# Optimization experiments

Hardware: AMD Instinct MI355X
Metric: run time of the kernel (lower is better)

## Reference

```python
import jax, jax.numpy as jnp
import numpy as np
from math import sqrt

HEADS = 16
DIM_HEAD = 64
BETA = 1.0 / sqrt(DIM_HEAD)


def setup_inputs() -> dict:
    key = jax.random.key(0)
    k1, k2, k3 = jax.random.split(key, 3)
    b, n, dim = 2, 2048, 1024
    inner = HEADS * DIM_HEAD  # 1024
    x = jax.random.normal(k1, (b, n, dim), dtype=jnp.float32)
    W_qk = jax.random.normal(k2, (dim, 2 * inner), dtype=jnp.float32) * 0.02
    W_out = jax.random.normal(k3, (inner, dim), dtype=jnp.float32) * 0.02
    return {"x": x, "W_qk": W_qk, "W_out": W_out}


def reference(x, W_qk, W_out):
    # x: [b, n, dim]; to_qk: Linear(dim, 2*inner, bias=False)
    b, n, _ = x.shape
    qk = x @ W_qk                                   # [b, n, 2*inner]
    q, k = jnp.split(qk, 2, axis=-1)                # each [b, n, inner]
    # b n (h d) -> b h n d
    q = q.reshape(b, n, HEADS, DIM_HEAD).transpose(0, 2, 1, 3)
    k = k.reshape(b, n, HEADS, DIM_HEAD).transpose(0, 2, 1, 3)
    # beta-scaled scores
    scores = jnp.einsum('bhid,bhjd->bhij', q * BETA, k)  # [b, h, n, n]
    mask_value = -jnp.finfo(scores.dtype).max
    causal_mask = jnp.triu(jnp.ones((n, n), dtype=bool), k=1)
    scores = jnp.where(causal_mask, mask_value, scores)
    attn = jax.nn.softmax(scores, axis=-1)
    # K is reused as V
    out = jnp.einsum('bhij,bhjd->bhid', attn, k)    # [b, h, n, d]
    out = out.transpose(0, 2, 1, 3).reshape(b, n, HEADS * DIM_HEAD)
    # to_out Linear (dropout is identity in eval)
    return out @ W_out
```

## Files before the change

kernel.cpp:

```cpp
#include <hip/hip_runtime.h>
#include <hip/hip_bf16.h>
#include <math.h>

typedef short bf16x8 __attribute__((ext_vector_type(8)));
typedef float f32x4 __attribute__((ext_vector_type(4)));

__device__ __forceinline__ float bf2f(unsigned short u) {
    return __uint_as_float(((unsigned int)u) << 16);
}
__device__ __forceinline__ unsigned short f2bf(float f) {
    unsigned int u = __float_as_uint(f);
    u = (u + 0x7FFFu + ((u >> 16) & 1u)) >> 16;
    return (unsigned short)u;
}
__device__ __forceinline__ unsigned int pk2bf(float a, float b) {
    __hip_bfloat162 u = __float22bfloat162_rn(make_float2(a, b));
    return *(unsigned int*)&u;
}

#define ASYNC16(gp, lp)                                                        \
    __builtin_amdgcn_global_load_lds(                                          \
        (const __attribute__((address_space(1))) unsigned int*)(gp),           \
        (__attribute__((address_space(3))) unsigned int*)(lp), 16, 0, 0)

__global__ __launch_bounds__(256) void wtrans_kernel(const float* __restrict__ Wqk,
                                                     const float* __restrict__ Wout,
                                                     unsigned short* __restrict__ Wqk_t,
                                                     unsigned short* __restrict__ Wout_t) {
    const int z = blockIdx.z;
    const int N = z ? 1024 : 2048;
    if (z && blockIdx.y >= 32) return;
    const float* in = z ? Wout : Wqk;
    unsigned short* out = z ? Wout_t : Wqk_t;
    const int K = 1024;
    __shared__ float tile[32][33];
    int k0 = blockIdx.x * 32, n0 = blockIdx.y * 32;
    int tx = threadIdx.x & 31, ty = threadIdx.x >> 5;
    #pragma unroll
    for (int i = ty; i < 32; i += 8)
        tile[i][tx] = in[(size_t)(k0 + i) * N + (n0 + tx)];
    __syncthreads();
    #pragma unroll
    for (int i = ty; i < 32; i += 8)
        out[(size_t)(n0 + i) * K + (k0 + tx)] = f2bf(tile[tx][i]);
}

template <bool STORE_BF16, bool A_FP32, bool WRITE_KT>
__global__ __launch_bounds__(256) void gemm12864_kernel(const void* __restrict__ Av,
                                                        const unsigned short* __restrict__ Bt,
                                                        void* __restrict__ C,
                                                        unsigned short* __restrict__ kT,
                                                        int K, int lda, int ldb, int ldc) {
    constexpr int ASTR = A_FP32 ? 40 : 32;
    __shared__ unsigned short As[128 * ASTR];
    __shared__ unsigned short Bs[64 * 32];
    const int tid = threadIdx.x;
    const int wave = tid >> 6;
    const int lane = tid & 63;
    const int quad = lane >> 4;
    const int col  = lane & 15;
    const int wm = (wave >> 1) * 64;
    const int wn = (wave & 1) * 32;
    const int m0 = blockIdx.x * 128, n0 = blockIdx.y * 64;

    f32x4 acc[4][2];
    #pragma unroll
    for (int i = 0; i < 4; ++i)
        #pragma unroll
        for (int j = 0; j < 2; ++j) { acc[i][j][0] = 0.f; acc[i][j][1] = 0.f; acc[i][j][2] = 0.f; acc[i][j][3] = 0.f; }

    const int srow = tid >> 2;
    const int skc  = (tid & 3) * 8;
    const int frow = tid >> 1;
    const int fcol = (tid & 1) * 16;

    for (int k0 = 0; k0 < K; k0 += 32) {
        __syncthreads();
        if (A_FP32) {
            const float* gx = (const float*)Av + (size_t)(m0 + frow) * lda + k0 + fcol;
            float4 f0 = *(const float4*)(gx);
            float4 f1 = *(const float4*)(gx + 4);
            float4 f2 = *(const float4*)(gx + 8);
            float4 f3 = *(const float4*)(gx + 12);
            uint4 w0 = make_uint4(pk2bf(f0.x, f0.y), pk2bf(f0.z, f0.w),
                                  pk2bf(f1.x, f1.y), pk2bf(f1.z, f1.w));
            uint4 w1 = make_uint4(pk2bf(f2.x, f2.y), pk2bf(f2.z, f2.w),
                                  pk2bf(f3.x, f3.y), pk2bf(f3.z, f3.w));
            *(uint4*)&As[frow * ASTR + fcol]     = w0;
            *(uint4*)&As[frow * ASTR + fcol + 8] = w1;
        } else {
            const unsigned short* ga = (const unsigned short*)Av + (size_t)(m0 + srow) * lda + k0 + skc;
            ASYNC16(ga,            &As[wave * 512]);
            ASYNC16(ga + 64 * lda, &As[2048 + wave * 512]);
        }
        const unsigned short* gb = Bt + (size_t)(n0 + srow) * ldb + k0 + skc;
        ASYNC16(gb, &Bs[wave * 512]);
        __syncthreads();

        bf16x8 af[4], bf[2];
        #pragma unroll
        for (int mf = 0; mf < 4; ++mf)
            af[mf] = *(const bf16x8*)&As[(wm + mf * 16 + col) * ASTR + quad * 8];
        #pragma unroll
        for (int nf = 0; nf < 2; ++nf)
            bf[nf] = *(const bf16x8*)&Bs[(wn + nf * 16 + col) * 32 + quad * 8];
        #pragma unroll
        for (int mf = 0; mf < 4; ++mf)
            #pragma unroll
            for (int nf = 0; nf < 2; ++nf)
                acc[mf][nf] = __builtin_amdgcn_mfma_f32_16x16x32_bf16(af[mf], bf[nf], acc[mf][nf], 0, 0, 0);
    }

    #pragma unroll
    for (int mf = 0; mf < 4; ++mf) {
        const int row0 = m0 + wm + mf * 16 + quad * 4;
        #pragma unroll
        for (int nf = 0; nf < 2; ++nf) {
            const int cc = n0 + wn + nf * 16 + col;
            #pragma unroll
            for (int r = 0; r < 4; ++r) {
                if (STORE_BF16)
                    ((unsigned short*)C)[(size_t)(row0 + r) * ldc + cc] = f2bf(acc[mf][nf][r]);
                else
                    ((float*)C)[(size_t)(row0 + r) * ldc + cc] = acc[mf][nf][r];
            }
            if (WRITE_KT && cc >= 1024) {
                const int bb = row0 >> 11, tok = row0 & 2047;
                ushort4 v;
                v.x = f2bf(acc[mf][nf][0]); v.y = f2bf(acc[mf][nf][1]);
                v.z = f2bf(acc[mf][nf][2]); v.w = f2bf(acc[mf][nf][3]);
                *(ushort4*)(kT + ((size_t)(bb * 1024 + cc - 1024)) * 2048 + tok) = v;
            }
        }
    }
}

#define LDK 72

__global__ __launch_bounds__(256) void attn_v5_kernel(const unsigned short* __restrict__ qkb,
                                                      const unsigned short* __restrict__ kT,
                                                      unsigned short* __restrict__ aout) {
    __shared__ unsigned short Kbuf[2][2][64 * 64];
    __shared__ unsigned short Ps[4][16 * LDK];

    const int bh = blockIdx.x;
    const int b = bh >> 4, h = bh & 15;
    const int qtile = 31 - (int)blockIdx.y;
    const int tid = threadIdx.x;
    const int wave = tid >> 6, lane = tid & 63, quad = lane >> 4, col = lane & 15;

    bf16x8 qa0, qa1;
    {
        const unsigned short* qp =
            qkb + ((size_t)(b * 2048 + qtile * 64 + wave * 16 + col)) * 2048 + h * 64;
        bf16x8 r0 = *(const bf16x8*)(qp + quad * 8);
        bf16x8 r1 = *(const bf16x8*)(qp + 32 + quad * 8);
        const float sc = 0.125f * 1.44269504088896f;
        #pragma unroll
        for (int i = 0; i < 8; ++i) {
            qa0[i] = (short)f2bf(bf2f((unsigned short)r0[i]) * sc);
            qa1[i] = (short)f2bf(bf2f((unsigned short)r1[i]) * sc);
        }
    }

    f32x4 accO[4];
    #pragma unroll
    for (int t = 0; t < 4; ++t) { accO[t][0] = 0.f; accO[t][1] = 0.f; accO[t][2] = 0.f; accO[t][3] = 0.f; }
    float lsum = 0.f;

    const int r8 = lane >> 3;
    const int c8 = (lane & 7) ^ r8;
    const unsigned short* knp =
        qkb + ((size_t)(b * 2048 + wave * 16 + r8)) * 2048 + 1024 + h * 64 + c8 * 8;
    const unsigned short* ktp = kT + ((size_t)(bh * 64 + wave * 16 + r8)) * 2048 + c8 * 8;

    auto issue = [&](int jt, int p) {
        const unsigned short* kn = knp + (size_t)jt * 64 * 2048;
        const unsigned short* kt = ktp + jt * 64;
        unsigned short* knl = &Kbuf[p][0][(wave * 16) * 64];
        unsigned short* ktl = &Kbuf[p][1][(wave * 16) * 64];
        ASYNC16(kn,            knl);
        ASYNC16(kn + 8 * 2048, knl + 8 * 64);
        ASYNC16(kt,            ktl);
        ASYNC16(kt + 8 * 2048, ktl + 8 * 64);
    };

    issue(0, 0);

    for (int jt = 0; jt <= qtile; ++jt) {
        const int cur = jt & 1;
        __builtin_amdgcn_s_barrier();
        if (jt < qtile) issue(jt + 1, cur ^ 1);
        if (jt < qtile) __builtin_amdgcn_s_waitcnt(0xF74);
        else            __builtin_amdgcn_s_waitcnt(0xF70);
        __builtin_amdgcn_s_barrier();
        __asm__ volatile("" ::: "memory");

        const unsigned short* Knc = &Kbuf[cur][0][0];
        const unsigned short* Ktc = &Kbuf[cur][1][0];

        const bool diag = (jt == qtile);
        const int tmax = diag ? wave : 3;

        float ls = 0.f;
        unsigned int pw[4][2];
        #pragma unroll
        for (int t = 0; t < 4; ++t) {
            if (t <= tmax) {
                const int row = (t * 16 + col) * 64;
                const int sw = col & 7;
                bf16x8 ka0 = *(const bf16x8*)&Knc[row + (quad ^ sw) * 8];
                bf16x8 ka1 = *(const bf16x8*)&Knc[row + ((4 + quad) ^ sw) * 8];
                f32x4 c = {-16.f, -16.f, -16.f, -16.f};
                c = __builtin_amdgcn_mfma_f32_16x16x32_bf16(ka0, qa0, c, 0, 0, 0);
                c = __builtin_amdgcn_mfma_f32_16x16x32_bf16(ka1, qa1, c, 0, 0, 0);
                if (diag && t == wave) {
                    #pragma unroll
                    for (int r = 0; r < 4; ++r)
                        if (quad * 4 + r > col) c[r] = -1e30f;
                }
                const float p0 = exp2f(c[0]);
                const float p1 = exp2f(c[1]);
                const float p2 = exp2f(c[2]);
                const float p3 = exp2f(c[3]);
                ls += (p0 + p1) + (p2 + p3);
                pw[t][0] = pk2bf(p0, p1);
                pw[t][1] = pk2bf(p2, p3);
            } else {
                pw[t][0] = 0u; pw[t][1] = 0u;
            }
        }
        lsum += ls;

        unsigned short* psb = &Ps[wave][col * LDK];
        #pragma unroll
        for (int t = 0; t < 4; ++t)
            *(uint2*)(psb + t * 16 + quad * 4) = make_uint2(pw[t][0], pw[t][1]);

        bf16x8 pa0 = *(const bf16x8*)(psb + quad * 8);
        bf16x8 pa1 = *(const bf16x8*)(psb + 32 + quad * 8);
        const bool hi = !(diag && wave < 2);

        #pragma unroll
        for (int t = 0; t < 4; ++t) {
            const int row = (t * 16 + col) * 64;
            const int sw = col & 7;
            bf16x8 vb0 = *(const bf16x8*)&Ktc[row + (quad ^ sw) * 8];
            accO[t] = __builtin_amdgcn_mfma_f32_16x16x32_bf16(pa0, vb0, accO[t], 0, 0, 0);
            if (hi) {
                bf16x8 vb1 = *(const bf16x8*)&Ktc[row + ((4 + quad) ^ sw) * 8];
                accO[t] = __builtin_amdgcn_mfma_f32_16x16x32_bf16(pa1, vb1, accO[t], 0, 0, 0);
            }
        }
    }

    lsum += __shfl_xor(lsum, 16);
    lsum += __shfl_xor(lsum, 32);
    #pragma unroll
    for (int r = 0; r < 4; ++r) {
        const float lr = __shfl(lsum, (lane & 48) | (quad * 4 + r));
        const float inv = 1.f / lr;
        const size_t row = (size_t)b * 2048 + qtile * 64 + wave * 16 + quad * 4 + r;
        unsigned short* op = aout + row * 1024 + h * 64;
        op[col]      = f2bf(accO[0][r] * inv);
        op[16 + col] = f2bf(accO[1][r] * inv);
        op[32 + col] = f2bf(accO[2][r] * inv);
        op[48 + col] = f2bf(accO[3][r] * inv);
    }
}

extern "C" void kernel_launch(void* const* d_in, const int* in_sizes, int n_in,
                              void* d_out, int out_size, void* d_ws, size_t ws_size,
                              hipStream_t stream) {
    (void)in_sizes; (void)n_in; (void)out_size; (void)ws_size;
    const float* x    = (const float*)d_in[0];
    const float* Wqk  = (const float*)d_in[1];
    const float* Wout = (const float*)d_in[2];
    float* out = (float*)d_out;

    unsigned short* kT     = (unsigned short*)d_ws;
    unsigned short* Wqk_t  = kT     + (size_t)2048 * 2048;
    unsigned short* Wout_t = Wqk_t  + (size_t)2048 * 1024;
    unsigned short* qkb    = Wout_t + (size_t)1024 * 1024;
    unsigned short* aoutb  = qkb    + (size_t)4096 * 2048;

    wtrans_kernel<<<dim3(32, 64, 2), dim3(256), 0, stream>>>(Wqk, Wout, Wqk_t, Wout_t);

    gemm12864_kernel<true, true, true><<<dim3(32, 32), dim3(256), 0, stream>>>(
        (const void*)x, Wqk_t, (void*)qkb, kT, 1024, 1024, 1024, 2048);

    attn_v5_kernel<<<dim3(32, 32), dim3(256), 0, stream>>>(qkb, kT, aoutb);

    gemm12864_kernel<false, false, false><<<dim3(32, 16), dim3(256), 0, stream>>>(
        (const void*)aoutb, Wout_t, (void*)out, nullptr, 1024, 1024, 1024, 1024);
}
```

Baseline: 198.3 us.

## Shrink GEMM tiles to 64x64 with register-staged loads and padded LDS

Replaces the 128x64 GEMM tile with a 64x64 tile in which each wave computes a 16x64 strip. Global loads are issued into registers before the barrier and then written to padded LDS (stride 40), replacing the async global-to-LDS path. This doubles the grid size for both projection GEMMs, aiming for better occupancy and latency hiding. In exchange, each MFMA gets less operand reuse and global/LDS traffic per FLOP rises.

```diff
diff --git a/kernel.cpp b/kernel.cpp
--- a/kernel.cpp
+++ b/kernel.cpp
@@ -46,91 +46,71 @@
 }
 
 template <bool STORE_BF16, bool A_FP32, bool WRITE_KT>
-__global__ __launch_bounds__(256) void gemm12864_kernel(const void* __restrict__ Av,
-                                                        const unsigned short* __restrict__ Bt,
-                                                        void* __restrict__ C,
-                                                        unsigned short* __restrict__ kT,
-                                                        int K, int lda, int ldb, int ldc) {
-    constexpr int ASTR = A_FP32 ? 40 : 32;
-    __shared__ unsigned short As[128 * ASTR];
-    __shared__ unsigned short Bs[64 * 32];
-    const int tid = threadIdx.x;
+__global__ __launch_bounds__(256) void gemm64_kernel(const void* __restrict__ Av,
+                                                     const unsigned short* __restrict__ Bt,
+                                                     void* __restrict__ C,
+                                                     unsigned short* __restrict__ kT,
+                                                     int K, int lda, int ldb, int ldc) {
+    __shared__ unsigned short As[64 * 40];
+    __shared__ unsigned short Bs[64 * 40];
+    const int tid  = threadIdx.x;
     const int wave = tid >> 6;
     const int lane = tid & 63;
     const int quad = lane >> 4;
-    const int col  = lane & 15;
-    const int wm = (wave >> 1) * 64;
-    const int wn = (wave & 1) * 32;
-    const int m0 = blockIdx.x * 128, n0 = blockIdx.y * 64;
-
-    f32x4 acc[4][2];
-    #pragma unroll
-    for (int i = 0; i < 4; ++i)
-        #pragma unroll
-        for (int j = 0; j < 2; ++j) { acc[i][j][0] = 0.f; acc[i][j][1] = 0.f; acc[i][j][2] = 0.f; acc[i][j][3] = 0.f; }
-
-    const int srow = tid >> 2;
-    const int skc  = (tid & 3) * 8;
-    const int frow = tid >> 1;
-    const int fcol = (tid & 1) * 16;
+    const int lrow = lane & 15;
+    const int m0 = blockIdx.x * 64;
+    const int n0 = blockIdx.y * 64;
+    const int ar = tid >> 2;
+    const int ac = (tid & 3) * 8;
+
+    f32x4 acc[4];
+    #pragma unroll
+    for (int t = 0; t < 4; ++t) { acc[t][0] = 0.f; acc[t][1] = 0.f; acc[t][2] = 0.f; acc[t][3] = 0.f; }
+
+    const unsigned short* Bp = Bt + (size_t)(n0 + ar) * ldb + ac;
 
     for (int k0 = 0; k0 < K; k0 += 32) {
-        __syncthreads();
+        bf16x8 bv = *(const bf16x8*)(Bp + k0);
         if (A_FP32) {
-            const float* gx = (const float*)Av + (size_t)(m0 + frow) * lda + k0 + fcol;
+            const float* gx = (const float*)Av + (size_t)(m0 + ar) * lda + k0 + ac;
             float4 f0 = *(const float4*)(gx);
             float4 f1 = *(const float4*)(gx + 4);
-            float4 f2 = *(const float4*)(gx + 8);
-            float4 f3 = *(const float4*)(gx + 12);
-            uint4 w0 = make_uint4(pk2bf(f0.x, f0.y), pk2bf(f0.z, f0.w),
-                                  pk2bf(f1.x, f1.y), pk2bf(f1.z, f1.w));
-            uint4 w1 = make_uint4(pk2bf(f2.x, f2.y), pk2bf(f2.z, f2.w),
-                                  pk2bf(f3.x, f3.y), pk2bf(f3.z, f3.w));
-            *(uint4*)&As[frow * ASTR + fcol]     = w0;
-            *(uint4*)&As[frow * ASTR + fcol + 8] = w1;
+            uint4 w = make_uint4(pk2bf(f0.x, f0.y), pk2bf(f0.z, f0.w),
+                                 pk2bf(f1.x, f1.y), pk2bf(f1.z, f1.w));
+            __syncthreads();
+            *(uint4*)&As[ar * 40 + ac] = w;
         } else {
-            const unsigned short* ga = (const unsigned short*)Av + (size_t)(m0 + srow) * lda + k0 + skc;
-            ASYNC16(ga,            &As[wave * 512]);
-            ASYNC16(ga + 64 * lda, &As[2048 + wave * 512]);
-        }
-        const unsigned short* gb = Bt + (size_t)(n0 + srow) * ldb + k0 + skc;
-        ASYNC16(gb, &Bs[wave * 512]);
+            bf16x8 av = *(const bf16x8*)((const unsigned short*)Av + (size_t)(m0 + ar) * lda + k0 + ac);
+            __syncthreads();
+            *(bf16x8*)&As[ar * 40 + ac] = av;
+        }
+        *(bf16x8*)&Bs[ar * 40 + ac] = bv;
         __syncthreads();
-
-        bf16x8 af[4], bf[2];
-        #pragma unroll
-        for (int mf = 0; mf < 4; ++mf)
-            af[mf] = *(const bf16x8*)&As[(wm + mf * 16 + col) * ASTR + quad * 8];
-        #pragma unroll
-        for (int nf = 0; nf < 2; ++nf)
-            bf[nf] = *(const bf16x8*)&Bs[(wn + nf * 16 + col) * 32 + quad * 8];
-        #pragma unroll
-        for (int mf = 0; mf < 4; ++mf)
-            #pragma unroll
-            for (int nf = 0; nf < 2; ++nf)
-                acc[mf][nf] = __builtin_amdgcn_mfma_f32_16x16x32_bf16(af[mf], bf[nf], acc[mf][nf], 0, 0, 0);
-    }
-
-    #pragma unroll
-    for (int mf = 0; mf < 4; ++mf) {
-        const int row0 = m0 + wm + mf * 16 + quad * 4;
-        #pragma unroll
-        for (int nf = 0; nf < 2; ++nf) {
-            const int cc = n0 + wn + nf * 16 + col;
-            #pragma unroll
-            for (int r = 0; r < 4; ++r) {
-                if (STORE_BF16)
-                    ((unsigned short*)C)[(size_t)(row0 + r) * ldc + cc] = f2bf(acc[mf][nf][r]);
-                else
-                    ((float*)C)[(size_t)(row0 + r) * ldc + cc] = acc[mf][nf][r];
-            }
-            if (WRITE_KT && cc >= 1024) {
-                const int bb = row0 >> 11, tok = row0 & 2047;
-                ushort4 v;
-                v.x = f2bf(acc[mf][nf][0]); v.y = f2bf(acc[mf][nf][1]);
-                v.z = f2bf(acc[mf][nf][2]); v.w = f2bf(acc[mf][nf][3]);
-                *(ushort4*)(kT + ((size_t)(bb * 1024 + cc - 1024)) * 2048 + tok) = v;
-            }
+        bf16x8 afrag = *(const bf16x8*)&As[(wave * 16 + lrow) * 40 + quad * 8];
+        #pragma unroll
+        for (int t = 0; t < 4; ++t) {
+            bf16x8 bfrag = *(const bf16x8*)&Bs[(t * 16 + lrow) * 40 + quad * 8];
+            acc[t] = __builtin_amdgcn_mfma_f32_16x16x32_bf16(afrag, bfrag, acc[t], 0, 0, 0);
+        }
+    }
+
+    const int row0 = m0 + wave * 16 + quad * 4;
+    #pragma unroll
+    for (int t = 0; t < 4; ++t) {
+        const int cc = n0 + t * 16 + lrow;
+        #pragma unroll
+        for (int r = 0; r < 4; ++r) {
+            if (STORE_BF16)
+                ((unsigned short*)C)[(size_t)(row0 + r) * ldc + cc] = f2bf(acc[t][r]);
+            else
+                ((float*)C)[(size_t)(row0 + r) * ldc + cc] = acc[t][r];
+        }
+        if (WRITE_KT && cc >= 1024) {
+            const int bb = row0 >> 11, tok = row0 & 2047;
+            ushort4 v;
+            v.x = f2bf(acc[t][0]); v.y = f2bf(acc[t][1]);
+            v.z = f2bf(acc[t][2]); v.w = f2bf(acc[t][3]);
+            *(ushort4*)(kT + ((size_t)(bb * 1024 + cc - 1024)) * 2048 + tok) = v;
         }
     }
 }
@@ -286,11 +266,11 @@
 
     wtrans_kernel<<<dim3(32, 64, 2), dim3(256), 0, stream>>>(Wqk, Wout, Wqk_t, Wout_t);
 
-    gemm12864_kernel<true, true, true><<<dim3(32, 32), dim3(256), 0, stream>>>(
+    gemm64_kernel<true, true, true><<<dim3(64, 32), dim3(256), 0, stream>>>(
         (const void*)x, Wqk_t, (void*)qkb, kT, 1024, 1024, 1024, 2048);
 
     attn_v5_kernel<<<dim3(32, 32), dim3(256), 0, stream>>>(qkb, kT, aoutb);
 
-    gemm12864_kernel<false, false, false><<<dim3(32, 16), dim3(256), 0, stream>>>(
+    gemm64_kernel<false, false, false><<<dim3(64, 16), dim3(256), 0, stream>>>(
         (const void*)aoutb, Wout_t, (void*)out, nullptr, 1024, 1024, 1024, 1024);
 }
```

Result: no change. 197.1 us (-0.6%).
